# Kernel optimization log

Measured on AMD Instinct MI355X. Metric: run time of the kernel, lower is better.

## Reference

```python
import jax, jax.numpy as jnp
import numpy as np

SEQ_LEN = 1
INPUT = 2048
HIDDEN = 2048
CLASSES = 10
K = int(np.floor(np.sqrt(HIDDEN)))            # avgKernelSize = 45
NUM_EH = (HIDDEN - K) // K + 1                # 45 pooled features
LENGTHS = (32, 128, 512)                      # EHlengths (window sizes)
EST_DIM = NUM_EH * len(LENGTHS) * 2           # mean + variance per (feature, window)
B = 8192


def setup_inputs() -> dict:
    key = jax.random.key(0)
    ks = jax.random.split(key, 7)
    s = 1.0 / np.sqrt(HIDDEN)
    u = lambda k, shape: jax.random.uniform(k, shape, jnp.float32, -s, s)
    return {
        "x": jax.random.normal(ks[0], (B, SEQ_LEN, INPUT), jnp.float32),
        "W_ih": u(ks[1], (HIDDEN, INPUT)),
        "W_hh": u(ks[2], (HIDDEN, HIDDEN)),
        "b_ih": u(ks[3], (HIDDEN,)),
        "b_hh": u(ks[4], (HIDDEN,)),
        "W_lin": u(ks[5], (CLASSES, HIDDEN + EST_DIM)),
        "b_lin": u(ks[6], (CLASSES,)),
    }


def _sliding_stats(pooled):
    """Causal sliding-window mean/variance over the batch/stream axis.

    pooled: (B, F). Returns (B, F, J, 2) with [..., 0]=mean, [..., 1]=var.
    This is the exact quantity the VarEH exponential histograms approximate
    (streaming mean/variance over the last L elements added).
    """
    n = pooled.shape[0]
    cs = jnp.cumsum(pooled, axis=0)
    cs2 = jnp.cumsum(pooled * pooled, axis=0)
    idx = jnp.arange(n)
    outs = []
    for L in LENGTHS:  # small fixed set of window lengths
        zpad = jnp.zeros((L,) + pooled.shape[1:], pooled.dtype)
        cs_l = jnp.concatenate([zpad, cs], axis=0)[:n]
        cs2_l = jnp.concatenate([zpad, cs2], axis=0)[:n]
        cnt = jnp.minimum(idx + 1, L).astype(pooled.dtype)[:, None]
        m = (cs - cs_l) / cnt
        v = (cs2 - cs2_l) / cnt - m * m
        outs.append(jnp.stack([m, v], axis=-1))  # (B, F, 2)
    return jnp.stack(outs, axis=2)  # (B, F, J, 2)


def reference(x, W_ih, W_hh, b_ih, b_hh, W_lin, b_lin):
    b = x.shape[0]
    # Elman RNN, batch_first, h0 = 0. Precompute input projection for all steps.
    xw = jnp.einsum("bsi,hi->bsh", x, W_ih) + b_ih + b_hh  # (B, S, H)

    def step(h, xt):
        h = jnp.tanh(xt + h @ W_hh.T)
        return h, h

    h0 = jnp.zeros((b, HIDDEN), x.dtype)
    _, hs = jax.lax.scan(step, h0, jnp.swapaxes(xw, 0, 1))  # (S, B, H)
    rnn_out = hs[-1]  # (B, H); with seq_len=1 this equals squeeze(rnn_out)

    # AvgPool1d(kernel=K, stride=K) over hidden dim -> (B, NUM_EH)
    pooled = rnn_out[:, : NUM_EH * K].reshape(b, NUM_EH, K).mean(axis=-1)

    # Streaming mean/var estimates across the batch stream (VarEH semantics)
    est = _sliding_stats(pooled).reshape(b, EST_DIM)

    lin_in = jnp.concatenate([rnn_out, est], axis=1)  # (B, H + EST_DIM)
    logits = lin_in @ W_lin.T + b_lin
    return jax.nn.softmax(logits, axis=1)
```

## Files before the change

### kernel.cpp

```cpp
#include <hip/hip_runtime.h>
#include <hip/hip_bf16.h>
#include <math.h>

typedef short s16x8 __attribute__((ext_vector_type(8)));
typedef float f32x4 __attribute__((ext_vector_type(4)));

__device__ inline unsigned short f2bf(float x) {
    unsigned int u = __float_as_uint(x);
    unsigned int r = (u + 0x7fffu + ((u >> 16) & 1u)) >> 16;
    return (unsigned short)r;
}
__device__ inline float bf2f(unsigned short u) {
    return __uint_as_float(((unsigned int)u) << 16);
}

__device__ inline float fast_tanh(float x) {
    float e = __expf(2.0f * x);
    return 1.0f - 2.0f * __builtin_amdgcn_rcpf(e + 1.0f);
}

__global__ void cvtprep_kernel(const float* __restrict__ x,
                               const float* __restrict__ W_ih,
                               const float* __restrict__ W_lin,
                               unsigned short* __restrict__ xb,
                               unsigned short* __restrict__ wb,
                               unsigned short* __restrict__ wlb,
                               float* __restrict__ zbase) {
    int blk = blockIdx.x;
    int tid = threadIdx.x;
    if (blk < 16384) {
        int i = blk * 256 + tid;
        float4 v = ((const float4*)x)[i];
        ushort4 o; o.x = f2bf(v.x); o.y = f2bf(v.y); o.z = f2bf(v.z); o.w = f2bf(v.w);
        ((ushort4*)xb)[i] = o;
    } else if (blk < 20480) {
        int i = (blk - 16384) * 256 + tid;
        float4 v = ((const float4*)W_ih)[i];
        ushort4 o; o.x = f2bf(v.x); o.y = f2bf(v.y); o.z = f2bf(v.z); o.w = f2bf(v.w);
        ((ushort4*)wb)[i] = o;
    } else if (blk < 20626) {
        int idx = (blk - 20480) * 256 + tid;
        int c = idx / 2336, k = idx - c * 2336;
        float v = (c < 10 && k < 2318) ? W_lin[c * 2318 + k] : 0.f;
        wlb[idx] = f2bf(v);
    } else {
        int i = (blk - 20626) * 256 + tid;
        ((float4*)zbase)[i] = float4{0.f, 0.f, 0.f, 0.f};
    }
}


#define MFMA_(a, b, c) __builtin_amdgcn_mfma_f32_16x16x32_bf16(a, b, c, 0, 0, 0)

__device__ inline s16x8 frag_ld(const unsigned short* hbase, int row, int ksub, int quad) {
    int slot = (ksub * 4 + quad) ^ (row & 7);
    return *(const s16x8*)(hbase + row * 64 + slot * 8);
}

__device__ inline void stage_u(const unsigned short* __restrict__ gmat, int half,
                               int rowoff, int kt, unsigned short* lmat, int tid) {
    int r = tid >> 3, s = tid & 7;
    int lr = rowoff + r;
    int ks = (s ^ (lr & 7)) << 3;
    const unsigned short* gp = gmat + (size_t)(half * 128 + lr) * 2048 + kt * 64 + ks;
    __builtin_amdgcn_global_load_lds(
        (const __attribute__((address_space(1))) void*)gp,
        (__attribute__((address_space(3))) void*)(lmat + half * 8192 + lr * 64 + s * 8),
        16, 0, 0);
}

#define LOAD_B(ks)                                                       \
    b0 = frag_ld(Bh, bco +  0 + mrow, (ks), quad);                       \
    b1 = frag_ld(Bh, bco + 16 + mrow, (ks), quad);                       \
    b2 = frag_ld(Bh, bco + 32 + mrow, (ks), quad);                       \
    b3 = frag_ld(Bh, bco + 48 + mrow, (ks), quad);

#define LOAD_A(h, ks)                                                    \
    af0 = frag_ld(Ah, (h) * 64 +  0 + mrow, (ks), quad);                 \
    af1 = frag_ld(Ah, (h) * 64 + 16 + mrow, (ks), quad);                 \
    af2 = frag_ld(Ah, (h) * 64 + 32 + mrow, (ks), quad);                 \
    af3 = frag_ld(Ah, (h) * 64 + 48 + mrow, (ks), quad);

#define MFMA_H(hh)                                                       \
    acc[(hh)*4 + 0][0] = MFMA_(af0, b0, acc[(hh)*4 + 0][0]);             \
    acc[(hh)*4 + 0][1] = MFMA_(af0, b1, acc[(hh)*4 + 0][1]);             \
    acc[(hh)*4 + 0][2] = MFMA_(af0, b2, acc[(hh)*4 + 0][2]);             \
    acc[(hh)*4 + 0][3] = MFMA_(af0, b3, acc[(hh)*4 + 0][3]);             \
    acc[(hh)*4 + 1][0] = MFMA_(af1, b0, acc[(hh)*4 + 1][0]);             \
    acc[(hh)*4 + 1][1] = MFMA_(af1, b1, acc[(hh)*4 + 1][1]);             \
    acc[(hh)*4 + 1][2] = MFMA_(af1, b2, acc[(hh)*4 + 1][2]);             \
    acc[(hh)*4 + 1][3] = MFMA_(af1, b3, acc[(hh)*4 + 1][3]);             \
    acc[(hh)*4 + 2][0] = MFMA_(af2, b0, acc[(hh)*4 + 2][0]);             \
    acc[(hh)*4 + 2][1] = MFMA_(af2, b1, acc[(hh)*4 + 2][1]);             \
    acc[(hh)*4 + 2][2] = MFMA_(af2, b2, acc[(hh)*4 + 2][2]);             \
    acc[(hh)*4 + 2][3] = MFMA_(af2, b3, acc[(hh)*4 + 2][3]);             \
    acc[(hh)*4 + 3][0] = MFMA_(af3, b0, acc[(hh)*4 + 3][0]);             \
    acc[(hh)*4 + 3][1] = MFMA_(af3, b1, acc[(hh)*4 + 3][1]);             \
    acc[(hh)*4 + 3][2] = MFMA_(af3, b2, acc[(hh)*4 + 3][2]);             \
    acc[(hh)*4 + 3][3] = MFMA_(af3, b3, acc[(hh)*4 + 3][3]);

#define PHASE_CORE(hh)                                                   \
    __builtin_amdgcn_s_barrier();                                        \
    asm volatile("s_waitcnt lgkmcnt(0)" ::: "memory");                   \
    __builtin_amdgcn_s_setprio(1);                                       \
    MFMA_H(hh);                                                          \
    __builtin_amdgcn_s_setprio(0);

__global__ __launch_bounds__(512) void gemm_tanh_kernel(
    const unsigned short* __restrict__ A, const unsigned short* __restrict__ Bm,
    const float* __restrict__ b_ih, const float* __restrict__ b_hh,
    const unsigned short* __restrict__ Wl,
    float* __restrict__ pooled_t, float* __restrict__ linp)
{
    __shared__ __align__(16) unsigned short lds[2][2][16384];

    const int tid  = threadIdx.x;
    const int lane = tid & 63;
    const int wave = tid >> 6;
    const int wgid = blockIdx.x;
    const int xcd  = wgid & 7;
    const int idx  = wgid >> 3;
    const int rblk = xcd * 4 + (idx & 3);
    const int cblk = idx >> 2;
    const int row0 = rblk * 256;
    const int col0 = cblk * 256;
    const int wm   = wave >> 2;
    const int wn   = wave & 3;
    const int quad = lane >> 4;
    const int mrow = lane & 15;
    const int NT   = 32;

    const unsigned short* Ag = A  + (size_t)row0 * 2048;
    const unsigned short* Bg = Bm + (size_t)col0 * 2048;

    f32x4 acc[8][4];
#pragma unroll
    for (int i = 0; i < 8; ++i)
#pragma unroll
        for (int j = 0; j < 4; ++j) acc[i][j] = f32x4{0.f, 0.f, 0.f, 0.f};

    stage_u(Ag, 0, 0,  0, lds[0][0], tid);  stage_u(Ag, 0, 64, 0, lds[0][0], tid);
    stage_u(Ag, 1, 0,  0, lds[0][0], tid);  stage_u(Ag, 1, 64, 0, lds[0][0], tid);
    stage_u(Bg, 0, 0,  0, lds[0][1], tid);  stage_u(Bg, 0, 64, 0, lds[0][1], tid);
    stage_u(Bg, 1, 0,  0, lds[0][1], tid);  stage_u(Bg, 1, 64, 0, lds[0][1], tid);
    stage_u(Bg, 0, 0,  1, lds[1][1], tid);  stage_u(Bg, 0, 64, 1, lds[1][1], tid);
    stage_u(Ag, 0, 0,  1, lds[1][0], tid);  stage_u(Ag, 1, 0,  1, lds[1][0], tid);
    asm volatile("s_waitcnt vmcnt(4)" ::: "memory");
    __builtin_amdgcn_s_barrier();

    for (int t = 0; t < NT; ++t) {
        const int buf = t & 1;
        unsigned short* LA  = lds[buf][0];
        unsigned short* LB  = lds[buf][1];
        unsigned short* NLA = lds[buf ^ 1][0];
        unsigned short* NLB = lds[buf ^ 1][1];
        const unsigned short* Ah = LA + wm * 8192;
        const unsigned short* Bh = LB + (wn >> 1) * 8192;
        const int bco = (wn & 1) * 64;

        s16x8 b0, b1, b2, b3;
        s16x8 af0, af1, af2, af3;

        LOAD_B(0);
        LOAD_A(0, 0);
        if (t + 1 < NT) {
            stage_u(Ag, 0, 64, t + 1, NLA, tid);
            stage_u(Ag, 1, 64, t + 1, NLA, tid);
            stage_u(Bg, 1, 0,  t + 1, NLB, tid);
            stage_u(Bg, 1, 64, t + 1, NLB, tid);
        }
        asm volatile("s_waitcnt lgkmcnt(4)" ::: "memory");
        PHASE_CORE(0);
        __builtin_amdgcn_s_barrier();

        LOAD_A(1, 0);
        PHASE_CORE(1);
        __builtin_amdgcn_s_barrier();

        LOAD_B(1);
        LOAD_A(0, 1);
        asm volatile("s_waitcnt lgkmcnt(4)" ::: "memory");
        PHASE_CORE(0);
        __builtin_amdgcn_s_barrier();

        LOAD_A(1, 1);
        if (t + 2 < NT) {
            stage_u(Bg, 0, 0,  t + 2, LB, tid);
            stage_u(Bg, 0, 64, t + 2, LB, tid);
            stage_u(Ag, 0, 0,  t + 2, LA, tid);
            stage_u(Ag, 1, 0,  t + 2, LA, tid);
        }
        PHASE_CORE(1);
        if (t + 2 < NT) {
            asm volatile("s_waitcnt vmcnt(4)" ::: "memory");
        } else if (t + 1 < NT) {
            asm volatile("s_waitcnt vmcnt(0)" ::: "memory");
        }
        __builtin_amdgcn_s_barrier();
    }

    __syncthreads();
    unsigned short* T = &lds[0][0][0];
    float bias[4];
#pragma unroll
    for (int j = 0; j < 4; ++j) {
        int gc = col0 + wn * 64 + j * 16 + mrow;
        bias[j] = b_ih[gc] + b_hh[gc];
    }
#pragma unroll
    for (int i = 0; i < 8; ++i) {
#pragma unroll
        for (int rr = 0; rr < 4; ++rr) {
            int lrow = wm * 128 + i * 16 + quad * 4 + rr;
#pragma unroll
            for (int j = 0; j < 4; ++j) {
                int lcol = wn * 64 + j * 16 + mrow;
                float v = acc[i][j][rr] + bias[j];
                int cb = (lcol >> 3) ^ (lrow & 7);
                T[lrow * 256 + cb * 8 + (lcol & 7)] = f2bf(fast_tanh(v));
            }
        }
    }
    __syncthreads();

    int f0 = col0 / 45;
    for (int o = tid; o < 1792; o += 512) {
        int lrow = o / 7;
        int fi = o - lrow * 7;
        int f = f0 + fi;
        if (f < 45) {
            int wsb = f * 45, web = wsb + 45;
            int s = (wsb > col0) ? wsb : col0;
            int e = (web < col0 + 256) ? web : (col0 + 256);
            if (s < e) {
                float sum = 0.f;
                for (int c = s - col0; c < e - col0; ++c) {
                    int cb = (c >> 3) ^ (lrow & 7);
                    sum += bf2f(T[lrow * 256 + cb * 8 + (c & 7)]);
                }
                atomicAdd(&pooled_t[f * 8192 + row0 + lrow], sum);
            }
        }
    }

    f32x4 la = f32x4{0.f, 0.f, 0.f, 0.f};
    f32x4 lb = f32x4{0.f, 0.f, 0.f, 0.f};
    const int lr0 = wave * 32 + mrow;
    const int lr1 = lr0 + 16;
#pragma unroll
    for (int ks = 0; ks < 8; ++ks) {
        int c = ks * 32 + quad * 8;
        s16x8 bfrag = *(const s16x8*)(Wl + (size_t)mrow * 2336 + col0 + c);
        int cb0 = (c >> 3) ^ (lr0 & 7);
        s16x8 a0 = *(const s16x8*)(T + lr0 * 256 + cb0 * 8);
        la = MFMA_(a0, bfrag, la);
        int cb1 = (c >> 3) ^ (lr1 & 7);
        s16x8 a1 = *(const s16x8*)(T + lr1 * 256 + cb1 * 8);
        lb = MFMA_(a1, bfrag, lb);
    }
    if (mrow < 10) {
#pragma unroll
        for (int rr = 0; rr < 4; ++rr) {
            atomicAdd(&linp[(size_t)(row0 + wave * 32 + quad * 4 + rr) * 10 + mrow], la[rr]);
            atomicAdd(&linp[(size_t)(row0 + wave * 32 + 16 + quad * 4 + rr) * 10 + mrow], lb[rr]);
        }
    }
}

__global__ __launch_bounds__(256) void scan_kernel(
    const float* __restrict__ pooled_t,
    float* __restrict__ cs_t, float* __restrict__ cs2_t,
    float* __restrict__ sums1, float* __restrict__ sums2) {
    __shared__ float t1[256], t2[256];
    int f  = blockIdx.x >> 3;
    int ch = blockIdx.x & 7;
    int tid = threadIdx.x;
    const float S = 1.0f / 45.0f;
    const float* p = pooled_t + f * 8192 + ch * 1024;
    float4 v = ((const float4*)p)[tid];
    v.x *= S; v.y *= S; v.z *= S; v.w *= S;
    float q1[4], q2[4];
    q1[0] = v.x;          q2[0] = v.x * v.x;
    q1[1] = q1[0] + v.y;  q2[1] = q2[0] + v.y * v.y;
    q1[2] = q1[1] + v.z;  q2[2] = q2[1] + v.z * v.z;
    q1[3] = q1[2] + v.w;  q2[3] = q2[2] + v.w * v.w;
    float s1 = q1[3], s2 = q2[3];
    t1[tid] = s1; t2[tid] = s2;
    __syncthreads();
    for (int d = 1; d < 256; d <<= 1) {
        float a1 = (tid >= d) ? t1[tid - d] : 0.f;
        float a2 = (tid >= d) ? t2[tid - d] : 0.f;
        __syncthreads();
        t1[tid] += a1; t2[tid] += a2;
        __syncthreads();
    }
    float r1 = t1[tid] - s1, r2 = t2[tid] - s2;
    float4 o1, o2;
    o1.x = r1 + q1[0]; o1.y = r1 + q1[1]; o1.z = r1 + q1[2]; o1.w = r1 + q1[3];
    o2.x = r2 + q2[0]; o2.y = r2 + q2[1]; o2.z = r2 + q2[2]; o2.w = r2 + q2[3];
    ((float4*)(cs_t  + f * 8192 + ch * 1024))[tid] = o1;
    ((float4*)(cs2_t + f * 8192 + ch * 1024))[tid] = o2;
    if (tid == 255) {
        sums1[f * 8 + ch] = t1[255];
        sums2[f * 8 + ch] = t2[255];
    }
}

#define ESTRIDE 290
__global__ __launch_bounds__(128) void final_kernel(
    const float* __restrict__ cs_t, const float* __restrict__ cs2_t,
    const float* __restrict__ sums1, const float* __restrict__ sums2,
    const unsigned short* __restrict__ Wb, const float* __restrict__ linp,
    const float* __restrict__ b_lin, float* __restrict__ out) {
    __shared__ unsigned short Es[32 * ESTRIDE];
    __shared__ float eb1[45 * 8], eb2[45 * 8];
    __shared__ float comb[2][16][17];
    int tid = threadIdx.x;
    int lane = tid & 63;
    int wave = tid >> 6;
    int b0 = blockIdx.x * 32;

    if (tid < 45) {
        float a = 0.f, b = 0.f;
#pragma unroll
        for (int c = 0; c < 8; ++c) {
            eb1[tid * 8 + c] = a; a += sums1[tid * 8 + c];
            eb2[tid * 8 + c] = b; b += sums2[tid * 8 + c];
        }
    }
    __syncthreads();

    for (int i = tid; i < 135 * 32; i += 128) {
        int fj = i >> 5, r = i & 31;
        int f = fj / 3, j = fj - 3 * f;
        int b = b0 + r;
        int L = (j == 0) ? 32 : (j == 1) ? 128 : 512;
        const float* c1 = cs_t + f * 8192;
        const float* c2 = cs2_t + f * 8192;
        float a1 = c1[b] + eb1[f * 8 + (b >> 10)];
        float a2 = c2[b] + eb2[f * 8 + (b >> 10)];
        float p1 = 0.f, p2 = 0.f;
        if (b >= L) {
            int ix = b - L;
            p1 = c1[ix] + eb1[f * 8 + (ix >> 10)];
            p2 = c2[ix] + eb2[f * 8 + (ix >> 10)];
        }
        float cnt = (float)((b + 1 < L) ? (b + 1) : L);
        float m = (a1 - p1) / cnt;
        float v = (a2 - p2) / cnt - m * m;
        int d0 = f * 6 + j * 2;
        Es[r * ESTRIDE + d0]     = f2bf(m);
        Es[r * ESTRIDE + d0 + 1] = f2bf(v);
    }
    for (int i = tid; i < 32 * 18; i += 128) {
        int r = i / 18, d = 270 + i % 18;
        Es[r * ESTRIDE + d] = 0;
    }
    __syncthreads();

    const int quad = lane >> 4;
    const int mrow = lane & 15;

    f32x4 acc = f32x4{0.f, 0.f, 0.f, 0.f};
    const unsigned short* erow = Es + (wave * 16 + mrow) * ESTRIDE + quad * 8;
    const unsigned short* wrow = Wb + (size_t)mrow * 2336 + 2048 + quad * 8;
#pragma unroll
    for (int k = 0; k < 288; k += 32) {
        s16x8 a = *(const s16x8*)(erow + k);
        s16x8 b = *(const s16x8*)(wrow + k);
        acc = __builtin_amdgcn_mfma_f32_16x16x32_bf16(a, b, acc, 0, 0, 0);
    }
#pragma unroll
    for (int r = 0; r < 4; ++r) comb[wave][quad * 4 + r][mrow] = acc[r];
    __syncthreads();

    if (tid < 32) {
        int w = tid >> 4, r = tid & 15;
        int grow = b0 + w * 16 + r;
        float lg[10];
        float mx = -1e30f;
#pragma unroll
        for (int c = 0; c < 10; ++c) {
            lg[c] = comb[w][r][c] + linp[(size_t)grow * 10 + c] + b_lin[c];
            mx = fmaxf(mx, lg[c]);
        }
        float s = 0.f;
#pragma unroll
        for (int c = 0; c < 10; ++c) { lg[c] = expf(lg[c] - mx); s += lg[c]; }
        float inv = 1.0f / s;
#pragma unroll
        for (int c = 0; c < 10; ++c) out[(size_t)grow * 10 + c] = lg[c] * inv;
    }
}

extern "C" void kernel_launch(void* const* d_in, const int* in_sizes, int n_in,
                              void* d_out, int out_size, void* d_ws, size_t ws_size,
                              hipStream_t stream) {
    const float* x     = (const float*)d_in[0];
    const float* W_ih  = (const float*)d_in[1];
    const float* b_ih  = (const float*)d_in[3];
    const float* b_hh  = (const float*)d_in[4];
    const float* W_lin = (const float*)d_in[5];
    const float* b_lin = (const float*)d_in[6];
    float* out = (float*)d_out;

    char* ws = (char*)d_ws;
    unsigned short* xb  = (unsigned short*)(ws);
    unsigned short* wb  = (unsigned short*)(ws + 33554432);
    float* pooled_t     = (float*)(ws + 41943040);
    float* linp         = (float*)(ws + 43417600);
    float* cs_t         = (float*)(ws + 43745280);
    float* cs2_t        = (float*)(ws + 45219840);
    unsigned short* wlb = (unsigned short*)(ws + 46694400);
    float* sums1        = (float*)(ws + 46769152);
    float* sums2        = (float*)(ws + 46770592);

    cvtprep_kernel<<<21066, 256, 0, stream>>>(x, W_ih, W_lin, xb, wb, wlb, pooled_t);
    gemm_tanh_kernel<<<256, 512, 0, stream>>>(xb, wb, b_ih, b_hh, wlb, pooled_t, linp);
    scan_kernel<<<360, 256, 0, stream>>>(pooled_t, cs_t, cs2_t, sums1, sums2);
    final_kernel<<<256, 128, 0, stream>>>(cs_t, cs2_t, sums1, sums2, wlb, linp, b_lin, out);
}
```

Baseline: 226.0 us.

## Fuse fp32-to-bf16 conversion of x into the GEMM A-tile load path

Removes the separate pass that converted the 64 MB fp32 input x to bf16 in workspace. The GEMM now loads fp32 x tiles into registers, converts them to bf16, and writes them swizzled into LDS, interleaved with the MFMA phases. This drops a full read plus write of the activation buffer and cuts the prep kernel's grid. In exchange, the GEMM reads twice as many bytes for A per tile, uses more VGPRs for staging, and needs retuned waitcnt values in its pipeline.

```diff
diff --git a/kernel.cpp b/kernel.cpp
--- a/kernel.cpp
+++ b/kernel.cpp
@@ -19,32 +19,27 @@
     return 1.0f - 2.0f * __builtin_amdgcn_rcpf(e + 1.0f);
 }
 
-__global__ void cvtprep_kernel(const float* __restrict__ x,
-                               const float* __restrict__ W_ih,
+__global__ void cvtprep_kernel(const float* __restrict__ W_ih,
                                const float* __restrict__ W_lin,
-                               unsigned short* __restrict__ xb,
                                unsigned short* __restrict__ wb,
                                unsigned short* __restrict__ wlb,
                                float* __restrict__ zbase) {
     int blk = blockIdx.x;
     int tid = threadIdx.x;
-    if (blk < 16384) {
+    if (blk < 4096) {
         int i = blk * 256 + tid;
-        float4 v = ((const float4*)x)[i];
-        ushort4 o; o.x = f2bf(v.x); o.y = f2bf(v.y); o.z = f2bf(v.z); o.w = f2bf(v.w);
-        ((ushort4*)xb)[i] = o;
-    } else if (blk < 20480) {
-        int i = (blk - 16384) * 256 + tid;
         float4 v = ((const float4*)W_ih)[i];
         ushort4 o; o.x = f2bf(v.x); o.y = f2bf(v.y); o.z = f2bf(v.z); o.w = f2bf(v.w);
         ((ushort4*)wb)[i] = o;
-    } else if (blk < 20626) {
-        int idx = (blk - 20480) * 256 + tid;
-        int c = idx / 2336, k = idx - c * 2336;
-        float v = (c < 10 && k < 2318) ? W_lin[c * 2318 + k] : 0.f;
-        wlb[idx] = f2bf(v);
+    } else if (blk < 4242) {
+        int idx = (blk - 4096) * 256 + tid;
+        if (idx < 37376) {
+            int c = idx / 2336, k = idx - c * 2336;
+            float v = (c < 10 && k < 2318) ? W_lin[c * 2318 + k] : 0.f;
+            wlb[idx] = f2bf(v);
+        }
     } else {
-        int i = (blk - 20626) * 256 + tid;
+        int i = (blk - 4242) * 256 + tid;
         ((float4*)zbase)[i] = float4{0.f, 0.f, 0.f, 0.f};
     }
 }
@@ -68,6 +63,40 @@
         (__attribute__((address_space(3))) void*)(lmat + half * 8192 + lr * 64 + s * 8),
         16, 0, 0);
 }
+
+#define ISSUE_A(kt)                                                          \
+    {                                                                        \
+        const float* g0 = Xg + (size_t)(      ar) * 2048 + (kt) * 64 + as * 8; \
+        const float* g1 = Xg + (size_t)(128 + ar) * 2048 + (kt) * 64 + as * 8; \
+        ra0 = *(const float4*)g0; ra1 = *(const float4*)(g0 + 4);            \
+        ra2 = *(const float4*)g1; ra3 = *(const float4*)(g1 + 4);            \
+        asm volatile("" ::: "memory");                                       \
+        const float* g2 = Xg + (size_t)( 64 + ar) * 2048 + (kt) * 64 + as * 8; \
+        const float* g3 = Xg + (size_t)(192 + ar) * 2048 + (kt) * 64 + as * 8; \
+        ra4 = *(const float4*)g2; ra5 = *(const float4*)(g2 + 4);            \
+        ra6 = *(const float4*)g3; ra7 = *(const float4*)(g3 + 4);            \
+    }
+
+#define CVT8(v, lo, hi)                                                      \
+    v[0] = f2bf(lo.x); v[1] = f2bf(lo.y); v[2] = f2bf(lo.z); v[3] = f2bf(lo.w); \
+    v[4] = f2bf(hi.x); v[5] = f2bf(hi.y); v[6] = f2bf(hi.z); v[7] = f2bf(hi.w);
+
+#define CVT_WRITE_TOP(dstA)                                                  \
+    {                                                                        \
+        s16x8 v0, v1;                                                        \
+        CVT8(v0, ra0, ra1); CVT8(v1, ra2, ra3);                              \
+        int off = ar * 64 + aslot * 8;                                       \
+        *(s16x8*)((dstA) + off) = v0;                                        \
+        *(s16x8*)((dstA) + 8192 + off) = v1;                                 \
+    }
+#define CVT_WRITE_BOT(dstA)                                                  \
+    {                                                                        \
+        s16x8 v0, v1;                                                        \
+        CVT8(v0, ra4, ra5); CVT8(v1, ra6, ra7);                              \
+        int off = (64 + ar) * 64 + aslot * 8;                                \
+        *(s16x8*)((dstA) + off) = v0;                                        \
+        *(s16x8*)((dstA) + 8192 + off) = v1;                                 \
+    }
 
 #define LOAD_B(ks)                                                       \
     b0 = frag_ld(Bh, bco +  0 + mrow, (ks), quad);                       \
@@ -107,7 +136,7 @@
     __builtin_amdgcn_s_setprio(0);
 
 __global__ __launch_bounds__(512) void gemm_tanh_kernel(
-    const unsigned short* __restrict__ A, const unsigned short* __restrict__ Bm,
+    const float* __restrict__ X, const unsigned short* __restrict__ Bm,
     const float* __restrict__ b_ih, const float* __restrict__ b_hh,
     const unsigned short* __restrict__ Wl,
     float* __restrict__ pooled_t, float* __restrict__ linp)
@@ -130,22 +159,30 @@
     const int mrow = lane & 15;
     const int NT   = 32;
 
-    const unsigned short* Ag = A  + (size_t)row0 * 2048;
+    const float* Xg = X + (size_t)row0 * 2048;
     const unsigned short* Bg = Bm + (size_t)col0 * 2048;
 
+    const int ar = tid >> 3;
+    const int as = tid & 7;
+    const int aslot = as ^ (ar & 7);
+    float4 ra0, ra1, ra2, ra3, ra4, ra5, ra6, ra7;
+
     f32x4 acc[8][4];
 #pragma unroll
     for (int i = 0; i < 8; ++i)
 #pragma unroll
         for (int j = 0; j < 4; ++j) acc[i][j] = f32x4{0.f, 0.f, 0.f, 0.f};
 
-    stage_u(Ag, 0, 0,  0, lds[0][0], tid);  stage_u(Ag, 0, 64, 0, lds[0][0], tid);
-    stage_u(Ag, 1, 0,  0, lds[0][0], tid);  stage_u(Ag, 1, 64, 0, lds[0][0], tid);
+    ISSUE_A(0);
     stage_u(Bg, 0, 0,  0, lds[0][1], tid);  stage_u(Bg, 0, 64, 0, lds[0][1], tid);
     stage_u(Bg, 1, 0,  0, lds[0][1], tid);  stage_u(Bg, 1, 64, 0, lds[0][1], tid);
+    asm volatile("s_waitcnt vmcnt(4)" ::: "memory");
+    CVT_WRITE_TOP(lds[0][0]);
+    CVT_WRITE_BOT(lds[0][0]);
+    ISSUE_A(1);
     stage_u(Bg, 0, 0,  1, lds[1][1], tid);  stage_u(Bg, 0, 64, 1, lds[1][1], tid);
-    stage_u(Ag, 0, 0,  1, lds[1][0], tid);  stage_u(Ag, 1, 0,  1, lds[1][0], tid);
-    asm volatile("s_waitcnt vmcnt(4)" ::: "memory");
+    asm volatile("s_waitcnt vmcnt(10)" ::: "memory");
+    asm volatile("s_waitcnt lgkmcnt(0)" ::: "memory");
     __builtin_amdgcn_s_barrier();
 
     for (int t = 0; t < NT; ++t) {
@@ -164,8 +201,6 @@
         LOAD_B(0);
         LOAD_A(0, 0);
         if (t + 1 < NT) {
-            stage_u(Ag, 0, 64, t + 1, NLA, tid);
-            stage_u(Ag, 1, 64, t + 1, NLA, tid);
             stage_u(Bg, 1, 0,  t + 1, NLB, tid);
             stage_u(Bg, 1, 64, t + 1, NLB, tid);
         }
@@ -174,12 +209,23 @@
         __builtin_amdgcn_s_barrier();
 
         LOAD_A(1, 0);
+        if (t + 1 < NT) {
+            asm volatile("s_waitcnt vmcnt(8)" ::: "memory");
+            CVT_WRITE_TOP(NLA);
+        }
         PHASE_CORE(1);
         __builtin_amdgcn_s_barrier();
 
         LOAD_B(1);
         LOAD_A(0, 1);
-        asm volatile("s_waitcnt lgkmcnt(4)" ::: "memory");
+        if (t + 1 < NT) {
+            asm volatile("s_waitcnt vmcnt(4)" ::: "memory");
+            CVT_WRITE_BOT(NLA);
+        }
+        if (t + 2 < NT) {
+            ISSUE_A(t + 2);
+        }
+        asm volatile("s_waitcnt lgkmcnt(2)" ::: "memory");
         PHASE_CORE(0);
         __builtin_amdgcn_s_barrier();
 
@@ -187,12 +233,10 @@
         if (t + 2 < NT) {
             stage_u(Bg, 0, 0,  t + 2, LB, tid);
             stage_u(Bg, 0, 64, t + 2, LB, tid);
-            stage_u(Ag, 0, 0,  t + 2, LA, tid);
-            stage_u(Ag, 1, 0,  t + 2, LA, tid);
         }
         PHASE_CORE(1);
         if (t + 2 < NT) {
-            asm volatile("s_waitcnt vmcnt(4)" ::: "memory");
+            asm volatile("s_waitcnt vmcnt(10)" ::: "memory");
         } else if (t + 1 < NT) {
             asm volatile("s_waitcnt vmcnt(0)" ::: "memory");
         }
@@ -405,18 +449,17 @@
     float* out = (float*)d_out;
 
     char* ws = (char*)d_ws;
-    unsigned short* xb  = (unsigned short*)(ws);
-    unsigned short* wb  = (unsigned short*)(ws + 33554432);
-    float* pooled_t     = (float*)(ws + 41943040);
-    float* linp         = (float*)(ws + 43417600);
-    float* cs_t         = (float*)(ws + 43745280);
-    float* cs2_t        = (float*)(ws + 45219840);
-    unsigned short* wlb = (unsigned short*)(ws + 46694400);
-    float* sums1        = (float*)(ws + 46769152);
-    float* sums2        = (float*)(ws + 46770592);
-
-    cvtprep_kernel<<<21066, 256, 0, stream>>>(x, W_ih, W_lin, xb, wb, wlb, pooled_t);
-    gemm_tanh_kernel<<<256, 512, 0, stream>>>(xb, wb, b_ih, b_hh, wlb, pooled_t, linp);
+    unsigned short* wb  = (unsigned short*)(ws);
+    float* pooled_t     = (float*)(ws + 8388608);
+    float* linp         = (float*)(ws + 9863168);
+    float* cs_t         = (float*)(ws + 10190848);
+    float* cs2_t        = (float*)(ws + 11665408);
+    unsigned short* wlb = (unsigned short*)(ws + 13139968);
+    float* sums1        = (float*)(ws + 13214720);
+    float* sums2        = (float*)(ws + 13216160);
+
+    cvtprep_kernel<<<4682, 256, 0, stream>>>(W_ih, W_lin, wb, wlb, pooled_t);
+    gemm_tanh_kernel<<<256, 512, 0, stream>>>(x, wb, b_ih, b_hh, wlb, pooled_t, linp);
     scan_kernel<<<360, 256, 0, stream>>>(pooled_t, cs_t, cs2_t, sums1, sums2);
     final_kernel<<<256, 128, 0, stream>>>(cs_t, cs2_t, sums1, sums2, wlb, linp, b_lin, out);
 }
```

Result: slower. 232.3 us (+2.8%).
